# Kernel optimization log

Measured on AMD Instinct MI355X. Metric: run time of the kernel, lower is better.

Reference implementation:

```python
import jax, jax.numpy as jnp
import numpy as np

IMG = 1024.0          # input image size (square)
PRE_NMS_TOPK = 1000   # per level (test-time)
POST_NMS_TOPK = 1000
NMS_THRESH = 0.7
MIN_BOX_SIZE = 0.0
A = 3                 # anchors (aspect ratios) per location
SIZES = [32, 64, 128, 256, 512]
STRIDES = [4, 8, 16, 32, 64]
FEATS = [256, 128, 64, 32, 16]
RATIOS = [0.5, 1.0, 2.0]
B = 8


def _make_anchors():
    out = []
    for size, stride, f in zip(SIZES, STRIDES, FEATS):
        base = np.stack([np.array([-size * np.sqrt(r) / 2, -size / np.sqrt(r) / 2,
                                   size * np.sqrt(r) / 2, size / np.sqrt(r) / 2])
                         for r in RATIOS])  # [A,4]
        c = (np.arange(f) + 0.5) * stride
        cx, cy = np.meshgrid(c, c)
        shifts = np.stack([cx.ravel(), cy.ravel(), cx.ravel(), cy.ravel()], 1)  # [f*f,4]
        anc = (shifts[:, None, :] + base[None, :, :]).reshape(-1, 4)  # [f*f*A,4]
        out.append(anc.astype(np.float32))
    return out


def setup_inputs() -> dict:
    key = jax.random.key(0)
    ancs = _make_anchors()
    inp = {}
    for i, (lvl, anc) in enumerate(zip(["p2", "p3", "p4", "p5", "p6"], ancs)):
        n = anc.shape[0]
        kd, kc = jax.random.split(jax.random.fold_in(key, i))
        # Box2BoxTransformLinear deltas: (l,t,r,b) distances normalized by anchor size
        inp[f"deltas_{lvl}"] = jax.random.uniform(kd, (B, n, 4), jnp.float32, 0.05, 0.6)
        inp[f"ctr_{lvl}"] = jax.random.normal(kc, (B, n), jnp.float32)
        inp[f"anchors_{lvl}"] = jnp.asarray(anc)
    return inp


def _decode_linear(deltas, anchors):
    # Box2BoxTransformLinear(normalize_by_size=True).apply_deltas
    x1, y1, x2, y2 = anchors[..., 0], anchors[..., 1], anchors[..., 2], anchors[..., 3]
    w, h = x2 - x1, y2 - y1
    cx, cy = (x1 + x2) * 0.5, (y1 + y2) * 0.5
    dl, dt, dr, db = deltas[..., 0], deltas[..., 1], deltas[..., 2], deltas[..., 3]
    return jnp.stack([cx - dl * w, cy - dt * h, cx + dr * w, cy + db * h], -1)


def _iou_matrix(b):
    area = jnp.clip(b[:, 2] - b[:, 0], 0.0) * jnp.clip(b[:, 3] - b[:, 1], 0.0)
    lt = jnp.maximum(b[:, None, :2], b[None, :, :2])
    rb = jnp.minimum(b[:, None, 2:], b[None, :, 2:])
    wh = jnp.clip(rb - lt, 0.0)
    inter = wh[..., 0] * wh[..., 1]
    return inter / (area[:, None] + area[None, :] - inter + 1e-8)


def _nms_one(args):
    boxes_off, boxes, scores = args  # [N,4],[N,4],[N]
    order = jnp.argsort(-scores)
    bo, b, s = boxes_off[order], boxes[order], scores[order]
    iou = _iou_matrix(jax.lax.stop_gradient(bo))  # keep mask is non-differentiable
    n = s.shape[0]
    idxs = jnp.arange(n)
    keep0 = s > -jnp.inf

    def body(i, keep):
        sup = (iou[i] > NMS_THRESH) & (idxs > i) & keep[i]
        return keep & (~sup)

    keep = jax.lax.fori_loop(0, n, body, keep0)
    s_keep = jnp.where(keep, s, -jnp.inf)
    top_s, top_i = jax.lax.top_k(s_keep, POST_NMS_TOPK)
    return b[top_i], top_s


def _forward(deltas_list, ctr_list, anchors_list):
    boxes_all, scores_all, lvl_all = [], [], []
    for li, (d, c, a) in enumerate(zip(deltas_list, ctr_list, anchors_list)):
        boxes = _decode_linear(d, a)               # [B,Ni,4]
        k = min(PRE_NMS_TOPK, c.shape[1])
        s_top, idx = jax.lax.top_k(c, k)           # per-image per-level topk
        boxes_top = jnp.take_along_axis(boxes, idx[:, :, None], axis=1)
        boxes_all.append(boxes_top)
        scores_all.append(s_top)
        lvl_all.append(jnp.full((k,), float(li), jnp.float32))
    boxes = jnp.concatenate(boxes_all, axis=1)     # [B,N,4]
    scores = jnp.concatenate(scores_all, axis=1)   # [B,N]
    lvl = jnp.concatenate(lvl_all)                 # [N]

    boxes = jnp.clip(boxes, 0.0, IMG)              # clip to image
    w = boxes[..., 2] - boxes[..., 0]
    h = boxes[..., 3] - boxes[..., 1]
    valid = (w > MIN_BOX_SIZE) & (h > MIN_BOX_SIZE)
    scores = jnp.where(valid, scores, -jnp.inf)
    # batched (per-level) NMS via coordinate offsets
    boxes_off = boxes + lvl[None, :, None] * (IMG + 1.0)

    out_boxes, out_scores = jax.lax.map(_nms_one, (boxes_off, boxes, scores))
    return jnp.concatenate([out_boxes, out_scores[..., None]], -1)  # [B,POST,5]


def reference(deltas_p2, deltas_p3, deltas_p4, deltas_p5, deltas_p6,
              ctr_p2, ctr_p3, ctr_p4, ctr_p5, ctr_p6,
              anchors_p2, anchors_p3, anchors_p4, anchors_p5, anchors_p6):
    return _forward([deltas_p2, deltas_p3, deltas_p4, deltas_p5, deltas_p6],
                    [ctr_p2, ctr_p3, ctr_p4, ctr_p5, ctr_p6],
                    [anchors_p2, anchors_p3, anchors_p4, anchors_p5, anchors_p6])
```

## Files before the change

### kernel.cpp

```cpp
#include <hip/hip_runtime.h>
#include <cstdint>
#include <cstddef>
#include <cmath>

#pragma clang fp contract(off)

namespace {

constexpr int kCandMax = 4096;

__device__ __constant__ int c_N[5] = {196608, 49152, 12288, 3072, 768};
__device__ __constant__ int c_K[5] = {1000, 1000, 1000, 1000, 768};

struct RPNParams {
  const float* deltas[5];
  const float* ctr[5];
  const float* anchors[5];
  float* scores;
  float* boxes;
  unsigned char* keep;
  unsigned int* mask;
  unsigned int* g0p;
  unsigned int* g1p;
  unsigned int* ccount;
  unsigned int* thresh;
  unsigned int* v0kk;
  unsigned long long* cand;
  float* out;
};

__device__ __forceinline__ unsigned int fkey(float f) {
  unsigned int u = __float_as_uint(f);
  return (u & 0x80000000u) ? ~u : (u | 0x80000000u);
}

__device__ __forceinline__ unsigned long long readlane64(unsigned long long v, int lane) {
  unsigned int lo = __builtin_amdgcn_readlane((unsigned int)v, lane);
  unsigned int hi = __builtin_amdgcn_readlane((unsigned int)(v >> 32), lane);
  return ((unsigned long long)hi << 32) | (unsigned long long)lo;
}

__global__ __launch_bounds__(256) void k_hist0(RPNParams P) {
  int bl = blockIdx.x, b = bl / 5, l = bl % 5;
  int N = c_N[l];
  int chunk = (N + 31) / 32;
  int i0 = blockIdx.y * chunk;
  int i1 = i0 + chunk; if (i1 > N) i1 = N;
  const float4* c4 = (const float4*)(P.ctr[l] + (size_t)b * N);
  __shared__ unsigned int wh[4][256];
  int tid = threadIdx.x, wid = tid >> 6;
  for (int i = tid; i < 1024; i += 256) ((unsigned int*)wh)[i] = 0u;
  __syncthreads();
  int q0 = i0 >> 2, q1 = i1 >> 2;
  for (int q = q0 + tid; q < q1; q += 256) {
    float4 v = c4[q];
    atomicAdd(&wh[wid][fkey(v.x) >> 24], 1u);
    atomicAdd(&wh[wid][fkey(v.y) >> 24], 1u);
    atomicAdd(&wh[wid][fkey(v.z) >> 24], 1u);
    atomicAdd(&wh[wid][fkey(v.w) >> 24], 1u);
  }
  __syncthreads();
  int bin = tid;
  P.g0p[((size_t)bl * 32 + blockIdx.y) * 256 + bin] =
      wh[0][bin] + wh[1][bin] + wh[2][bin] + wh[3][bin];
}

__global__ __launch_bounds__(256) void k_sum0(RPNParams P) {
  int bl = blockIdx.x;
  int K = c_K[bl % 5];
  __shared__ unsigned int S[257];
  int tid = threadIdx.x;
  unsigned int s = 0;
  const unsigned int* base = P.g0p + (size_t)bl * 32 * 256 + tid;
  #pragma unroll 8
  for (int p = 0; p < 32; ++p) s += base[p * 256];
  S[tid] = s;
  if (tid == 0) S[256] = 0u;
  __syncthreads();
  for (int d = 1; d < 256; d <<= 1) {
    unsigned int v = (tid + d < 256) ? S[tid + d] : 0u;
    __syncthreads();
    S[tid] += v;
    __syncthreads();
  }
  if (tid == 0) {
    int lo = 0, hi = 255;
    while (lo < hi) { int mid = (lo + hi + 1) >> 1; if (S[mid] >= (unsigned int)K) lo = mid; else hi = mid - 1; }
    P.v0kk[bl * 2] = (unsigned int)lo;
    P.v0kk[bl * 2 + 1] = (unsigned int)K - S[lo + 1];
  }
}

__global__ __launch_bounds__(256) void k_hist1(RPNParams P) {
  int bl = blockIdx.x, b = bl / 5, l = bl % 5;
  int N = c_N[l];
  int chunk = (N + 31) / 32;
  int i0 = blockIdx.y * chunk;
  int i1 = i0 + chunk; if (i1 > N) i1 = N;
  const float4* c4 = (const float4*)(P.ctr[l] + (size_t)b * N);
  unsigned int v0 = P.v0kk[bl * 2];
  __shared__ unsigned int wh[4][256];
  int tid = threadIdx.x, wid = tid >> 6;
  for (int i = tid; i < 1024; i += 256) ((unsigned int*)wh)[i] = 0u;
  __syncthreads();
  int q0 = i0 >> 2, q1 = i1 >> 2;
  for (int q = q0 + tid; q < q1; q += 256) {
    float4 v = c4[q];
    unsigned int u0 = fkey(v.x), u1 = fkey(v.y), u2 = fkey(v.z), u3 = fkey(v.w);
    if ((u0 >> 24) == v0) atomicAdd(&wh[wid][(u0 >> 16) & 255u], 1u);
    if ((u1 >> 24) == v0) atomicAdd(&wh[wid][(u1 >> 16) & 255u], 1u);
    if ((u2 >> 24) == v0) atomicAdd(&wh[wid][(u2 >> 16) & 255u], 1u);
    if ((u3 >> 24) == v0) atomicAdd(&wh[wid][(u3 >> 16) & 255u], 1u);
  }
  __syncthreads();
  int bin = tid;
  P.g1p[((size_t)bl * 32 + blockIdx.y) * 256 + bin] =
      wh[0][bin] + wh[1][bin] + wh[2][bin] + wh[3][bin];
}

__global__ __launch_bounds__(256) void k_thresh(RPNParams P) {
  int bl = blockIdx.x;
  __shared__ unsigned int S[257];
  int tid = threadIdx.x;
  if (tid == 0) P.ccount[bl * 256] = 0u;
  unsigned int s = 0;
  const unsigned int* base = P.g1p + (size_t)bl * 32 * 256 + tid;
  #pragma unroll 8
  for (int p = 0; p < 32; ++p) s += base[p * 256];
  S[tid] = s;
  if (tid == 0) S[256] = 0u;
  __syncthreads();
  for (int d = 1; d < 256; d <<= 1) {
    unsigned int v = (tid + d < 256) ? S[tid + d] : 0u;
    __syncthreads();
    S[tid] += v;
    __syncthreads();
  }
  if (tid == 0) {
    unsigned int kk = P.v0kk[bl * 2 + 1];
    unsigned int v0 = P.v0kk[bl * 2];
    int lo = 0, hi = 255;
    while (lo < hi) { int mid = (lo + hi + 1) >> 1; if (S[mid] >= kk) lo = mid; else hi = mid - 1; }
    P.thresh[bl] = ((v0 << 8) | (unsigned int)lo) << 16;
  }
}

__global__ __launch_bounds__(256) void k_compact(RPNParams P) {
  int bl = blockIdx.x, b = bl / 5, l = bl % 5;
  int N = c_N[l];
  int chunk = (N + 31) / 32;
  int i0 = blockIdx.y * chunk;
  int i1 = i0 + chunk; if (i1 > N) i1 = N;
  const float4* c4 = (const float4*)(P.ctr[l] + (size_t)b * N);
  unsigned int T = P.thresh[bl];
  unsigned long long* cand = P.cand + (size_t)bl * kCandMax;
  __shared__ unsigned int wcnt[4], wbase[4];
  int tid = threadIdx.x, lane = tid & 63, wid = tid >> 6;
  int q0 = i0 >> 2, q1 = i1 >> 2;
  unsigned int cnt = 0;
  for (int q = q0 + tid; q < q1; q += 256) {
    float4 v = c4[q];
    cnt += (fkey(v.x) >= T) + (fkey(v.y) >= T) + (fkey(v.z) >= T) + (fkey(v.w) >= T);
  }
  for (int d = 32; d > 0; d >>= 1) cnt += (unsigned int)__shfl_xor((int)cnt, d, 64);
  if (lane == 0) wcnt[wid] = cnt;
  __syncthreads();
  if (tid == 0) {
    unsigned int tot = wcnt[0] + wcnt[1] + wcnt[2] + wcnt[3];
    unsigned int base = tot ? atomicAdd(&P.ccount[bl * 256], tot) : 0u;
    unsigned int acc = base;
    for (int w = 0; w < 4; ++w) { unsigned int x = wcnt[w]; wbase[w] = acc; acc += x; }
  }
  __syncthreads();
  unsigned int off = wbase[wid];
  unsigned long long lmlt = (1ull << lane) - 1ull;
  for (int q = q0 + tid; q < q1; q += 256) {
    float4 v = c4[q];
    unsigned int u[4] = {fkey(v.x), fkey(v.y), fkey(v.z), fkey(v.w)};
    #pragma unroll
    for (int k = 0; k < 4; ++k) {
      bool pred = (u[k] >= T);
      unsigned long long m = __ballot(pred);
      if (pred) {
        unsigned int pos = off + (unsigned int)__popcll(m & lmlt);
        if (pos < (unsigned int)kCandMax) {
          unsigned int idx = (unsigned int)(q * 4 + k);
          cand[pos] = ((unsigned long long)u[k] << 32) |
                      (unsigned long long)(0xFFFFFFFFu - idx);
        }
      }
      off += (unsigned int)__popcll(m);
    }
  }
}

__global__ __launch_bounds__(1024) void k_select(RPNParams P) {
  int bl = blockIdx.x, b = bl / 5, l = bl % 5;
  int N = c_N[l], K = c_K[l];
  const float* ctr = P.ctr[l] + (size_t)b * N;
  __shared__ unsigned long long cand[kCandMax];
  int tid = threadIdx.x;
  int cc = (int)P.ccount[bl * 256]; if (cc > kCandMax) cc = kCandMax;
  const unsigned long long* gc = P.cand + (size_t)bl * kCandMax;
  for (int i = tid; i < cc; i += 1024) cand[i] = gc[i];
  int n2 = 1; while (n2 < cc) n2 <<= 1;
  for (int i = cc + tid; i < n2; i += 1024) cand[i] = 0ull;
  __syncthreads();
  for (int size = 2; size <= n2; size <<= 1) {
    for (int stride = size >> 1; stride > 0; stride >>= 1) {
      for (int i = tid; i < n2; i += 1024) {
        int j = i ^ stride;
        if (j > i) {
          unsigned long long a = cand[i], c2 = cand[j];
          bool sw = ((i & size) == 0) ? (a < c2) : (a > c2);
          if (sw) { cand[i] = c2; cand[j] = a; }
        }
      }
      __syncthreads();
    }
  }
  size_t sbase = ((size_t)b * 5 + l) * 1024;
  for (int r = tid; r < K; r += 1024) {
    unsigned long long cv = cand[r];
    unsigned int idx = 0xFFFFFFFFu - (unsigned int)(cv & 0xFFFFFFFFu);
    float s = ctr[idx];
    float4 anc = *(const float4*)(P.anchors[l] + (size_t)idx * 4);
    float4 dd  = *(const float4*)(P.deltas[l] + ((size_t)b * N + idx) * 4);
    float w = anc.z - anc.x, hgt = anc.w - anc.y;
    float cx = (anc.x + anc.z) * 0.5f, cy = (anc.y + anc.w) * 0.5f;
    float x1 = cx - dd.x * w;
    float y1 = cy - dd.y * hgt;
    float x2 = cx + dd.z * w;
    float y2 = cy + dd.w * hgt;
    x1 = fminf(fmaxf(x1, 0.0f), 1024.0f);
    y1 = fminf(fmaxf(y1, 0.0f), 1024.0f);
    x2 = fminf(fmaxf(x2, 0.0f), 1024.0f);
    y2 = fminf(fmaxf(y2, 0.0f), 1024.0f);
    bool valid = ((x2 - x1) > 0.0f) && ((y2 - y1) > 0.0f);
    P.scores[sbase + r] = valid ? s : -INFINITY;
    *(float4*)(P.boxes + (sbase + r) * 4) = make_float4(x1, y1, x2, y2);
  }
}

__global__ __launch_bounds__(256) void k_mask(RPNParams P) {
  int bl = blockIdx.x, b = bl / 5, l = bl % 5;
  int K = c_K[l];
  int tid = threadIdx.x;
  int lane = tid & 63;
  int yg = blockIdx.y * 4 + (tid >> 6);
  int zc = blockIdx.z;
  float off = (float)l * 1025.0f;
  size_t sbase = ((size_t)b * 5 + l) * 1024;
  __shared__ alignas(16) float4 obox[1024];
  __shared__ float area[1024];
  for (int i = tid; i < 1024; i += 256) {
    float4 v = make_float4(0.f, 0.f, 0.f, 0.f);
    if (i < K) {
      v = ((const float4*)P.boxes)[sbase + i];
      v.x += off; v.y += off; v.z += off; v.w += off;
    }
    obox[i] = v;
    area[i] = fmaxf(v.z - v.x, 0.0f) * fmaxf(v.w - v.y, 0.0f);
  }
  __syncthreads();
  int i = yg * 64 + lane;
  if (i >= K) return;
  float4 bi = obox[i];
  float ai = area[i];
  unsigned int* mrow = P.mask + (sbase + (size_t)i) * 32;
  const double M = 0x1.666667p-1;
  auto pr = [&](int j) -> bool {
    float4 bj = obox[j];
    float aj = area[j];
    float xx1 = fmaxf(bi.x, bj.x);
    float yy1 = fmaxf(bi.y, bj.y);
    float xx2 = fminf(bi.z, bj.z);
    float yy2 = fminf(bi.w, bj.w);
    float ww = fmaxf(xx2 - xx1, 0.0f);
    float hh = fmaxf(yy2 - yy1, 0.0f);
    float inter = ww * hh;
    float uni = ai + aj - inter + 1e-8f;
    return (double)inter >= M * (double)uni;
  };
  int wown = 2 * yg;
  if (zc == 0) {
    for (int w = 0; w < wown; ++w) mrow[w] = 0u;
    unsigned int m0, m1;
    if (lane < 32) { m0 = (1u << lane) - 1u; m1 = 0u; }
    else           { m0 = 0xFFFFFFFFu; m1 = (1u << (lane - 32)) - 1u; }
    #pragma unroll
    for (int h = 0; h < 2; ++h) {
      unsigned int bits = 0u;
      int j0 = (wown + h) << 5;
      for (int jj = 0; jj < 32; ++jj)
        if (pr(j0 + jj)) bits |= (1u << jj);
      mrow[wown + h] = bits & (h ? m1 : m0);
    }
  }
  int wstart = wown + 2;
  int nw = 32 - wstart;
  int qlen = (nw + 7) >> 3;
  int wbeg = wstart + zc * qlen;
  int wend = wbeg + qlen; if (wend > 32) wend = 32;
  for (int w = wbeg; w < wend; ++w) {
    unsigned int bits = 0u;
    int j0 = w << 5;
    for (int jj = 0; jj < 32; ++jj)
      if (pr(j0 + jj)) bits |= (1u << jj);
    mrow[w] = bits;
  }
}

__global__ __launch_bounds__(1024) void k_sweep(RPNParams P) {
  int bl = blockIdx.x, b = bl / 5, l = bl % 5;
  int K = c_K[l];
  int NW = (K + 63) >> 6;
  size_t sbase = ((size_t)b * 5 + l) * 1024;
  __shared__ alignas(16) unsigned long long lmask[16 * 1000];
  __shared__ unsigned long long rdiag[1024];
  __shared__ unsigned long long svalid[16];
  __shared__ unsigned long long skept[16];
  int tid = threadIdx.x;
  const ulonglong2* gm2 = (const ulonglong2*)(P.mask + sbase * 32);
  for (int j = tid; j < K * 8; j += 1024) {
    ulonglong2 v = gm2[j];
    ((ulonglong2*)lmask)[j] = v;
    int w0i = j * 2;
    int row = w0i >> 4;
    int dcol = row >> 6;
    int col0 = w0i & 15;
    if (col0 == dcol) rdiag[row] = v.x;
    else if (col0 + 1 == dcol) rdiag[row] = v.y;
  }
  __syncthreads();
  if (tid >= 64) return;
  int lane = tid;
  for (int g = 0; g < NW; ++g) {
    int e = g * 64 + lane;
    bool pred = (e < K) && (P.scores[sbase + e] > -INFINITY);
    unsigned long long m = __ballot(pred);
    if (lane == 0) svalid[g] = m;
  }
  int sub = lane >> 4, col = lane & 15;
  unsigned long long accA = 0ull, accB = 0ull;
  for (int g = 0; g < NW; ++g) {
    unsigned long long am = accA | accB;
    unsigned long long suppr = readlane64(am, g) | readlane64(am, g + 16) |
                               readlane64(am, g + 32) | readlane64(am, g + 48);
    unsigned long long A = svalid[g] & ~suppr;
    unsigned long long colmask = rdiag[g * 64 + lane];
    unsigned long long kept = 0ull;
    while (A) {
      bool cand = (A >> lane) & 1ull;
      unsigned long long D = __ballot(cand && ((colmask & A) == 0ull));
      kept |= D;
      unsigned long long sup = __ballot((colmask & D) != 0ull);
      A &= ~(D | sup);
    }
    if (lane == 0) skept[g] = kept;
    const unsigned long long* rowbase = &lmask[((size_t)g * 64 + (size_t)sub) * 16 + col];
    #pragma unroll
    for (int t = 0; t < 8; ++t) {
      int p0 = (2 * t) * 4 + sub;
      int p1 = (2 * t + 1) * 4 + sub;
      unsigned long long s0 = 0ull - ((kept >> p0) & 1ull);
      unsigned long long s1 = 0ull - ((kept >> p1) & 1ull);
      accA |= rowbase[(size_t)(2 * t) * 64] & s0;
      accB |= rowbase[(size_t)(2 * t + 1) * 64] & s1;
    }
  }
  for (int g = 0; g < NW; ++g) {
    unsigned long long kv = skept[g];
    int e = g * 64 + lane;
    if (e < K) P.keep[sbase + e] = (unsigned char)((kv >> lane) & 1ull);
  }
}

__global__ __launch_bounds__(1024) void k_merge(RPNParams P) {
  int b = blockIdx.x;
  __shared__ unsigned long long keyL[5][1000];
  __shared__ unsigned short srt[4768];
  __shared__ unsigned int wsum[16];
  __shared__ unsigned int sTot;
  int tid = threadIdx.x;
  int lane = tid & 63, wid = tid >> 6;

  for (int l = 0; l < 5; ++l) {
    int Kl = c_K[l];
    int r = tid;
    bool active = r < Kl;
    unsigned long long k = 0ull;
    bool flag = false;
    if (active) {
      float s = P.scores[((size_t)b * 5 + l) * 1024 + r];
      unsigned int fk = fkey(s);
      flag = fk > 0x007FFFFFu;
      unsigned int cidx = (unsigned int)(l * 1000 + r);
      k = ((unsigned long long)fk << 32) |
          (unsigned long long)(0xFFFFFFFFu - cidx);
    }
    unsigned int fv = flag ? 1u : 0u;
    unsigned int v = fv;
    for (int d = 1; d < 64; d <<= 1) {
      unsigned int n = __shfl_up(v, (unsigned int)d, 64);
      if (lane >= d) v += n;
    }
    if (lane == 63) wsum[wid] = v;
    __syncthreads();
    if (tid == 0) {
      unsigned int acc = 0;
      for (int w = 0; w < 16; ++w) { unsigned int x = wsum[w]; wsum[w] = acc; acc += x; }
      sTot = acc;
    }
    __syncthreads();
    unsigned int excl = wsum[wid] + (v - fv);
    unsigned int nValid = sTot;
    if (active) {
      unsigned int dest = flag ? excl : (nValid + ((unsigned int)r - excl));
      keyL[l][dest] = k;
    }
    __syncthreads();
  }

  for (int e = tid; e < 4768; e += 1024) {
    int l = (e < 4000) ? (e / 1000) : 4;
    int p = e - l * 1000;
    unsigned long long k = keyL[l][p];
    int rank = p;
    #pragma unroll
    for (int l2 = 0; l2 < 5; ++l2) {
      if (l2 == l) continue;
      int lo = 0, hi = c_K[l2];
      while (lo < hi) {
        int mid = (lo + hi) >> 1;
        if (keyL[l2][mid] > k) lo = mid + 1; else hi = mid;
      }
      rank += lo;
    }
    srt[rank] = (unsigned short)(0xFFFFFFFFu - (unsigned int)(k & 0xFFFFFFFFu));
  }
  __syncthreads();

  int base = tid * 5;
  unsigned char lf[5];
  unsigned short lc[5];
  unsigned int lsum = 0;
  for (int q = 0; q < 5; ++q) {
    int i = base + q;
    unsigned char f = 0; unsigned short cx = 0;
    if (i < 4768) {
      cx = srt[i];
      int l = cx / 1000;
      int r = (int)cx - l * 1000;
      f = P.keep[((size_t)b * 5 + l) * 1024 + r];
    }
    lf[q] = f; lc[q] = cx; lsum += f;
  }
  unsigned int v = lsum;
  for (int d = 1; d < 64; d <<= 1) {
    unsigned int n = __shfl_up(v, (unsigned int)d, 64);
    if (lane >= d) v += n;
  }
  if (lane == 63) wsum[wid] = v;
  __syncthreads();
  if (tid == 0) {
    unsigned int acc = 0;
    for (int w = 0; w < 16; ++w) { unsigned int x = wsum[w]; wsum[w] = acc; acc += x; }
    sTot = acc;
  }
  __syncthreads();
  unsigned int excl = wsum[wid] + (v - lsum);
  unsigned int tot = sTot;
  for (int q = 0; q < 5; ++q) {
    int i = base + q;
    if (i >= 4768) break;
    unsigned int cidx = (unsigned int)lc[q];
    int l = (int)(cidx / 1000u);
    int r = (int)cidx - l * 1000;
    size_t sb = ((size_t)b * 5 + l) * 1024 + r;
    unsigned char f = lf[q];
    unsigned int pos = f ? excl : (tot + ((unsigned int)i - excl));
    excl += f;
    if (pos < 1000u) {
      float4 bx = ((const float4*)P.boxes)[sb];
      float sc = f ? P.scores[sb] : -INFINITY;
      float* o = P.out + ((size_t)b * 1000 + pos) * 5;
      o[0] = bx.x; o[1] = bx.y; o[2] = bx.z; o[3] = bx.w; o[4] = sc;
    }
  }
}

}

extern "C" void kernel_launch(void* const* d_in, const int* in_sizes, int n_in,
                              void* d_out, int out_size, void* d_ws, size_t ws_size,
                              hipStream_t stream) {
  (void)out_size; (void)ws_size;
  RPNParams P;
  bool interleaved = (n_in >= 3) && (in_sizes[2] == 786432);
  for (int l = 0; l < 5; ++l) {
    if (interleaved) {
      P.deltas[l]  = (const float*)d_in[3 * l + 0];
      P.ctr[l]     = (const float*)d_in[3 * l + 1];
      P.anchors[l] = (const float*)d_in[3 * l + 2];
    } else {
      P.deltas[l]  = (const float*)d_in[l];
      P.ctr[l]     = (const float*)d_in[5 + l];
      P.anchors[l] = (const float*)d_in[10 + l];
    }
  }
  char* ws = (char*)d_ws;
  P.scores = (float*)(ws + 0);
  P.boxes  = (float*)(ws + 163840);
  P.keep   = (unsigned char*)(ws + 819200);
  P.mask   = (unsigned int*)(ws + 860160);
  P.cand   = (unsigned long long*)(ws + 860160);
  P.g0p    = (unsigned int*)(ws + 2170880);
  P.g1p    = (unsigned int*)(ws + 3481600);
  P.ccount = (unsigned int*)(ws + 6103040);
  P.thresh = (unsigned int*)(ws + 6144000);
  P.v0kk   = (unsigned int*)(ws + 6144160);
  P.out    = (float*)d_out;

  hipLaunchKernelGGL(k_hist0, dim3(40, 32), dim3(256), 0, stream, P);
  hipLaunchKernelGGL(k_sum0, dim3(40), dim3(256), 0, stream, P);
  hipLaunchKernelGGL(k_hist1, dim3(40, 32), dim3(256), 0, stream, P);
  hipLaunchKernelGGL(k_thresh, dim3(40), dim3(256), 0, stream, P);
  hipLaunchKernelGGL(k_compact, dim3(40, 32), dim3(256), 0, stream, P);
  hipLaunchKernelGGL(k_select, dim3(40), dim3(1024), 0, stream, P);
  hipLaunchKernelGGL(k_mask, dim3(40, 4, 8), dim3(256), 0, stream, P);
  hipLaunchKernelGGL(k_sweep, dim3(40), dim3(1024), 0, stream, P);
  hipLaunchKernelGGL(k_merge, dim3(8), dim3(1024), 0, stream, P);
}
```

Baseline: 118.7 us.

## Fold histogram reductions into consumer kernels and precompute merge keys in select

```diff
diff --git a/kernel.cpp b/kernel.cpp
--- a/kernel.cpp
+++ b/kernel.cpp
@@ -23,9 +23,9 @@
   unsigned int* g0p;
   unsigned int* g1p;
   unsigned int* ccount;
-  unsigned int* thresh;
   unsigned int* v0kk;
   unsigned long long* cand;
+  unsigned long long* keyC;
   float* out;
 };
 
@@ -49,6 +49,7 @@
   const float4* c4 = (const float4*)(P.ctr[l] + (size_t)b * N);
   __shared__ unsigned int wh[4][256];
   int tid = threadIdx.x, wid = tid >> 6;
+  if (blockIdx.y == 0 && tid == 0) P.ccount[bl * 256] = 0u;
   for (int i = tid; i < 1024; i += 256) ((unsigned int*)wh)[i] = 0u;
   __syncthreads();
   int q0 = i0 >> 2, q1 = i1 >> 2;
@@ -65,17 +66,24 @@
       wh[0][bin] + wh[1][bin] + wh[2][bin] + wh[3][bin];
 }
 
-__global__ __launch_bounds__(256) void k_sum0(RPNParams P) {
-  int bl = blockIdx.x;
-  int K = c_K[bl % 5];
+__global__ __launch_bounds__(256) void k_hist1(RPNParams P) {
+  int bl = blockIdx.x, b = bl / 5, l = bl % 5;
+  int N = c_N[l], K = c_K[l];
+  int chunk = (N + 31) / 32;
+  int i0 = blockIdx.y * chunk;
+  int i1 = i0 + chunk; if (i1 > N) i1 = N;
+  const float4* c4 = (const float4*)(P.ctr[l] + (size_t)b * N);
   __shared__ unsigned int S[257];
-  int tid = threadIdx.x;
-  unsigned int s = 0;
-  const unsigned int* base = P.g0p + (size_t)bl * 32 * 256 + tid;
-  #pragma unroll 8
-  for (int p = 0; p < 32; ++p) s += base[p * 256];
-  S[tid] = s;
-  if (tid == 0) S[256] = 0u;
+  __shared__ unsigned int wh[4][256];
+  int tid = threadIdx.x, wid = tid >> 6;
+  {
+    unsigned int s = 0;
+    const unsigned int* base0 = P.g0p + (size_t)bl * 32 * 256 + tid;
+    #pragma unroll 8
+    for (int p = 0; p < 32; ++p) s += base0[p * 256];
+    S[tid] = s;
+    if (tid == 0) S[256] = 0u;
+  }
   __syncthreads();
   for (int d = 1; d < 256; d <<= 1) {
     unsigned int v = (tid + d < 256) ? S[tid + d] : 0u;
@@ -83,24 +91,13 @@
     S[tid] += v;
     __syncthreads();
   }
-  if (tid == 0) {
-    int lo = 0, hi = 255;
-    while (lo < hi) { int mid = (lo + hi + 1) >> 1; if (S[mid] >= (unsigned int)K) lo = mid; else hi = mid - 1; }
-    P.v0kk[bl * 2] = (unsigned int)lo;
+  int lo = 0, hi = 255;
+  while (lo < hi) { int mid = (lo + hi + 1) >> 1; if (S[mid] >= (unsigned int)K) lo = mid; else hi = mid - 1; }
+  unsigned int v0 = (unsigned int)lo;
+  if (blockIdx.y == 0 && tid == 0) {
+    P.v0kk[bl * 2] = v0;
     P.v0kk[bl * 2 + 1] = (unsigned int)K - S[lo + 1];
   }
-}
-
-__global__ __launch_bounds__(256) void k_hist1(RPNParams P) {
-  int bl = blockIdx.x, b = bl / 5, l = bl % 5;
-  int N = c_N[l];
-  int chunk = (N + 31) / 32;
-  int i0 = blockIdx.y * chunk;
-  int i1 = i0 + chunk; if (i1 > N) i1 = N;
-  const float4* c4 = (const float4*)(P.ctr[l] + (size_t)b * N);
-  unsigned int v0 = P.v0kk[bl * 2];
-  __shared__ unsigned int wh[4][256];
-  int tid = threadIdx.x, wid = tid >> 6;
   for (int i = tid; i < 1024; i += 256) ((unsigned int*)wh)[i] = 0u;
   __syncthreads();
   int q0 = i0 >> 2, q1 = i1 >> 2;
@@ -118,33 +115,6 @@
       wh[0][bin] + wh[1][bin] + wh[2][bin] + wh[3][bin];
 }
 
-__global__ __launch_bounds__(256) void k_thresh(RPNParams P) {
-  int bl = blockIdx.x;
-  __shared__ unsigned int S[257];
-  int tid = threadIdx.x;
-  if (tid == 0) P.ccount[bl * 256] = 0u;
-  unsigned int s = 0;
-  const unsigned int* base = P.g1p + (size_t)bl * 32 * 256 + tid;
-  #pragma unroll 8
-  for (int p = 0; p < 32; ++p) s += base[p * 256];
-  S[tid] = s;
-  if (tid == 0) S[256] = 0u;
-  __syncthreads();
-  for (int d = 1; d < 256; d <<= 1) {
-    unsigned int v = (tid + d < 256) ? S[tid + d] : 0u;
-    __syncthreads();
-    S[tid] += v;
-    __syncthreads();
-  }
-  if (tid == 0) {
-    unsigned int kk = P.v0kk[bl * 2 + 1];
-    unsigned int v0 = P.v0kk[bl * 2];
-    int lo = 0, hi = 255;
-    while (lo < hi) { int mid = (lo + hi + 1) >> 1; if (S[mid] >= kk) lo = mid; else hi = mid - 1; }
-    P.thresh[bl] = ((v0 << 8) | (unsigned int)lo) << 16;
-  }
-}
-
 __global__ __launch_bounds__(256) void k_compact(RPNParams P) {
   int bl = blockIdx.x, b = bl / 5, l = bl % 5;
   int N = c_N[l];
@@ -152,10 +122,29 @@
   int i0 = blockIdx.y * chunk;
   int i1 = i0 + chunk; if (i1 > N) i1 = N;
   const float4* c4 = (const float4*)(P.ctr[l] + (size_t)b * N);
-  unsigned int T = P.thresh[bl];
   unsigned long long* cand = P.cand + (size_t)bl * kCandMax;
+  __shared__ unsigned int S[257];
   __shared__ unsigned int wcnt[4], wbase[4];
   int tid = threadIdx.x, lane = tid & 63, wid = tid >> 6;
+  {
+    unsigned int s = 0;
+    const unsigned int* base1 = P.g1p + (size_t)bl * 32 * 256 + tid;
+    #pragma unroll 8
+    for (int p = 0; p < 32; ++p) s += base1[p * 256];
+    S[tid] = s;
+    if (tid == 0) S[256] = 0u;
+  }
+  __syncthreads();
+  for (int d = 1; d < 256; d <<= 1) {
+    unsigned int v = (tid + d < 256) ? S[tid + d] : 0u;
+    __syncthreads();
+    S[tid] += v;
+    __syncthreads();
+  }
+  unsigned int v0 = P.v0kk[bl * 2], kk = P.v0kk[bl * 2 + 1];
+  int lo = 0, hi = 255;
+  while (lo < hi) { int mid = (lo + hi + 1) >> 1; if (S[mid] >= kk) lo = mid; else hi = mid - 1; }
+  unsigned int T = ((v0 << 8) | (unsigned int)lo) << 16;
   int q0 = i0 >> 2, q1 = i1 >> 2;
   unsigned int cnt = 0;
   for (int q = q0 + tid; q < q1; q += 256) {
@@ -199,7 +188,10 @@
   int N = c_N[l], K = c_K[l];
   const float* ctr = P.ctr[l] + (size_t)b * N;
   __shared__ unsigned long long cand[kCandMax];
+  __shared__ unsigned int wsum[16];
+  __shared__ unsigned int sTot;
   int tid = threadIdx.x;
+  int lane = tid & 63, wid = tid >> 6;
   int cc = (int)P.ccount[bl * 256]; if (cc > kCandMax) cc = kCandMax;
   const unsigned long long* gc = P.cand + (size_t)bl * kCandMax;
   for (int i = tid; i < cc; i += 1024) cand[i] = gc[i];
@@ -220,7 +212,10 @@
     }
   }
   size_t sbase = ((size_t)b * 5 + l) * 1024;
-  for (int r = tid; r < K; r += 1024) {
+  int r = tid;
+  unsigned long long kc = 0ull;
+  bool flag = false;
+  if (r < K) {
     unsigned long long cv = cand[r];
     unsigned int idx = 0xFFFFFFFFu - (unsigned int)(cv & 0xFFFFFFFFu);
     float s = ctr[idx];
@@ -237,8 +232,32 @@
     x2 = fminf(fmaxf(x2, 0.0f), 1024.0f);
     y2 = fminf(fmaxf(y2, 0.0f), 1024.0f);
     bool valid = ((x2 - x1) > 0.0f) && ((y2 - y1) > 0.0f);
-    P.scores[sbase + r] = valid ? s : -INFINITY;
+    float sc = valid ? s : -INFINITY;
+    P.scores[sbase + r] = sc;
     *(float4*)(P.boxes + (sbase + r) * 4) = make_float4(x1, y1, x2, y2);
+    unsigned int fk = fkey(sc);
+    flag = fk > 0x007FFFFFu;
+    unsigned int cidx = (unsigned int)(l * 1000 + r);
+    kc = ((unsigned long long)fk << 32) |
+         (unsigned long long)(0xFFFFFFFFu - cidx);
+  }
+  unsigned int fv = flag ? 1u : 0u, v = fv;
+  for (int d = 1; d < 64; d <<= 1) {
+    unsigned int n = __shfl_up(v, (unsigned int)d, 64);
+    if (lane >= d) v += n;
+  }
+  if (lane == 63) wsum[wid] = v;
+  __syncthreads();
+  if (tid == 0) {
+    unsigned int acc = 0;
+    for (int w = 0; w < 16; ++w) { unsigned int x = wsum[w]; wsum[w] = acc; acc += x; }
+    sTot = acc;
+  }
+  __syncthreads();
+  unsigned int excl = wsum[wid] + (v - fv);
+  if (r < K) {
+    unsigned int dest = flag ? excl : (sTot + ((unsigned int)r - excl));
+    P.keyC[(size_t)bl * 1024 + dest] = kc;
   }
 }
 
@@ -299,7 +318,7 @@
   }
   int wstart = wown + 2;
   int nw = 32 - wstart;
-  int qlen = (nw + 7) >> 3;
+  int qlen = (nw + 15) >> 4;
   int wbeg = wstart + zc * qlen;
   int wend = wbeg + qlen; if (wend > 32) wend = 32;
   for (int w = wbeg; w < wend; ++w) {
@@ -332,15 +351,16 @@
     if (col0 == dcol) rdiag[row] = v.x;
     else if (col0 + 1 == dcol) rdiag[row] = v.y;
   }
+  {
+    int g = tid >> 6;
+    int e = g * 64 + (tid & 63);
+    bool pred = (e < K) && (P.scores[sbase + e] > -INFINITY);
+    unsigned long long m = __ballot(pred);
+    if ((tid & 63) == 0) svalid[g] = m;
+  }
   __syncthreads();
   if (tid >= 64) return;
   int lane = tid;
-  for (int g = 0; g < NW; ++g) {
-    int e = g * 64 + lane;
-    bool pred = (e < K) && (P.scores[sbase + e] > -INFINITY);
-    unsigned long long m = __ballot(pred);
-    if (lane == 0) svalid[g] = m;
-  }
   int sub = lane >> 4, col = lane & 15;
   unsigned long long accA = 0ull, accB = 0ull;
   for (int g = 0; g < NW; ++g) {
@@ -385,42 +405,10 @@
   int tid = threadIdx.x;
   int lane = tid & 63, wid = tid >> 6;
 
-  for (int l = 0; l < 5; ++l) {
-    int Kl = c_K[l];
-    int r = tid;
-    bool active = r < Kl;
-    unsigned long long k = 0ull;
-    bool flag = false;
-    if (active) {
-      float s = P.scores[((size_t)b * 5 + l) * 1024 + r];
-      unsigned int fk = fkey(s);
-      flag = fk > 0x007FFFFFu;
-      unsigned int cidx = (unsigned int)(l * 1000 + r);
-      k = ((unsigned long long)fk << 32) |
-          (unsigned long long)(0xFFFFFFFFu - cidx);
-    }
-    unsigned int fv = flag ? 1u : 0u;
-    unsigned int v = fv;
-    for (int d = 1; d < 64; d <<= 1) {
-      unsigned int n = __shfl_up(v, (unsigned int)d, 64);
-      if (lane >= d) v += n;
-    }
-    if (lane == 63) wsum[wid] = v;
-    __syncthreads();
-    if (tid == 0) {
-      unsigned int acc = 0;
-      for (int w = 0; w < 16; ++w) { unsigned int x = wsum[w]; wsum[w] = acc; acc += x; }
-      sTot = acc;
-    }
-    __syncthreads();
-    unsigned int excl = wsum[wid] + (v - fv);
-    unsigned int nValid = sTot;
-    if (active) {
-      unsigned int dest = flag ? excl : (nValid + ((unsigned int)r - excl));
-      keyL[l][dest] = k;
-    }
-    __syncthreads();
-  }
+  #pragma unroll
+  for (int l = 0; l < 5; ++l)
+    if (tid < c_K[l]) keyL[l][tid] = P.keyC[((size_t)b * 5 + l) * 1024 + tid];
+  __syncthreads();
 
   for (int e = tid; e < 4768; e += 1024) {
     int l = (e < 4000) ? (e / 1000) : 4;
@@ -518,17 +506,15 @@
   P.g0p    = (unsigned int*)(ws + 2170880);
   P.g1p    = (unsigned int*)(ws + 3481600);
   P.ccount = (unsigned int*)(ws + 6103040);
-  P.thresh = (unsigned int*)(ws + 6144000);
-  P.v0kk   = (unsigned int*)(ws + 6144160);
+  P.v0kk   = (unsigned int*)(ws + 6144000);
+  P.keyC   = (unsigned long long*)(ws + 6144320);
   P.out    = (float*)d_out;
 
   hipLaunchKernelGGL(k_hist0, dim3(40, 32), dim3(256), 0, stream, P);
-  hipLaunchKernelGGL(k_sum0, dim3(40), dim3(256), 0, stream, P);
   hipLaunchKernelGGL(k_hist1, dim3(40, 32), dim3(256), 0, stream, P);
-  hipLaunchKernelGGL(k_thresh, dim3(40), dim3(256), 0, stream, P);
   hipLaunchKernelGGL(k_compact, dim3(40, 32), dim3(256), 0, stream, P);
   hipLaunchKernelGGL(k_select, dim3(40), dim3(1024), 0, stream, P);
-  hipLaunchKernelGGL(k_mask, dim3(40, 4, 8), dim3(256), 0, stream, P);
+  hipLaunchKernelGGL(k_mask, dim3(40, 4, 16), dim3(256), 0, stream, P);
   hipLaunchKernelGGL(k_sweep, dim3(40), dim3(1024), 0, stream, P);
   hipLaunchKernelGGL(k_merge, dim3(8), dim3(1024), 0, stream, P);
 }
```

Result: faster. 113.1 us (-4.7%).
